# Performance work log

Hardware: AMD Instinct MI355X
Metric: run time of the kernel (lower is better)

The kernel has to match this reference:

```python
import jax, jax.numpy as jnp
import numpy as np

N, L, HH, WW, E, NH = 8, 300, 96, 96, 256, 8


def setup_inputs() -> dict:
    key = jax.random.key(0)
    ks = jax.random.split(key, 9)
    return {
        "query_row": jax.random.normal(ks[0], (N, L, E), dtype=jnp.float32),
        "query_col": jax.random.normal(ks[1], (N, L, E), dtype=jnp.float32),
        "key_row": jax.random.normal(ks[2], (N, HH, WW, E), dtype=jnp.float32),
        "key_col": jax.random.normal(ks[3], (N, HH, WW, E), dtype=jnp.float32),
        "value": jax.random.normal(ks[4], (N, HH, WW, E), dtype=jnp.float32),
        "in_proj_weight": jax.random.normal(ks[5], (5 * E, E), dtype=jnp.float32) * 0.02,
        "in_proj_bias": jax.random.normal(ks[6], (5 * E,), dtype=jnp.float32) * 0.02,
        "out_proj_weight": jax.random.normal(ks[7], (E, E), dtype=jnp.float32) * 0.02,
        "out_proj_bias": jax.random.normal(ks[8], (E,), dtype=jnp.float32) * 0.02,
        "num_heads": NH,
    }


def reference(query_row, query_col, key_row, key_col, value,
              in_proj_weight, in_proj_bias, out_proj_weight, out_proj_bias,
              num_heads):
    bsz, tgt_len, embed_dim = query_row.shape
    head_dim = embed_dim // num_heads
    scaling = float(head_dim) ** -0.5

    def proj(x, i):
        w = in_proj_weight[i * embed_dim:(i + 1) * embed_dim]
        b = in_proj_bias[i * embed_dim:(i + 1) * embed_dim]
        return x @ w.T + b

    q_row = proj(query_row, 0) * scaling          # (N, L, E)
    q_col = proj(query_col, 1) * scaling          # (N, L, E)
    k_row = proj(key_row, 2).mean(axis=1)         # mean over H -> (N, W, E)
    k_col = proj(key_col, 3).mean(axis=2)         # mean over W -> (N, H, E)
    v = proj(value, 4)                            # (N, H, W, E)

    heads = lambda t: t.reshape(*t.shape[:-1], num_heads, head_dim)
    qr, qc, kr, kc = heads(q_row), heads(q_col), heads(k_row), heads(k_col)
    vh = heads(v)                                 # (N, H, W, nh, hd)

    # additive row/col decomposed scores -> independent softmaxes
    w_row = jax.nn.softmax(jnp.einsum('blnd,bwnd->bnlw', qr, kr), axis=-1)  # (N,nh,L,W)
    w_col = jax.nn.softmax(jnp.einsum('blnd,bhnd->bnlh', qc, kc), axis=-1)  # (N,nh,L,H)

    # contract col weights with value over H, then row weights over W
    tmp = jnp.einsum('bnlh,bhwnd->bnlwd', w_col, vh)       # (N,nh,L,W,hd)
    out = jnp.einsum('bnlw,bnlwd->blnd', w_row, tmp)       # (N,L,nh,hd)
    out = out.reshape(bsz, tgt_len, embed_dim).transpose(1, 0, 2)  # (L,N,E)
    return out @ out_proj_weight.T + out_proj_bias
```

## Files before the change

kernel.cpp:

```cpp
#include <hip/hip_runtime.h>
#include <cstdint>


typedef __attribute__((ext_vector_type(8))) short short8v;
typedef __attribute__((ext_vector_type(4))) short short4v;
typedef __attribute__((ext_vector_type(4))) float f32x4;

#define SCALE_Q 0.17677669529663687f

#define GLL16(gp, lp)                                                   \
  __builtin_amdgcn_global_load_lds(                                     \
      (const __attribute__((address_space(1))) void*)(gp),              \
      (__attribute__((address_space(3))) void*)(lp), 16, 0, 0)

__device__ __forceinline__ unsigned short f2bf(float x) {
  unsigned int u = __builtin_bit_cast(unsigned int, x);
  u += 0x7FFFu + ((u >> 16) & 1u);
  return (unsigned short)(u >> 16);
}

__device__ __forceinline__ unsigned int cvtpk(float a, float b) {
  unsigned int r;
  asm("v_cvt_pk_bf16_f32 %0, %1, %2" : "=v"(r) : "v"(a), "v"(b));
  return r;
}

__device__ __forceinline__ short8v pack8cvt(const f32x4& lo, const f32x4& hi) {
  union { short8v s; unsigned int u[4]; } z;
  z.u[0] = cvtpk(lo[0], lo[1]);
  z.u[1] = cvtpk(lo[2], lo[3]);
  z.u[2] = cvtpk(hi[0], hi[1]);
  z.u[3] = cvtpk(hi[2], hi[3]);
  return z.s;
}

__device__ __forceinline__ short4v pack4cvt(float a, float b, float c, float d) {
  union { short4v s; unsigned int u[2]; } z;
  z.u[0] = cvtpk(a, b);
  z.u[1] = cvtpk(c, d);
  return z.s;
}

__device__ __forceinline__ short8v pack8(const float4& fa, const float4& fb) {
  short8v v;
  v[0] = (short)f2bf(fa.x); v[1] = (short)f2bf(fa.y);
  v[2] = (short)f2bf(fa.z); v[3] = (short)f2bf(fa.w);
  v[4] = (short)f2bf(fb.x); v[5] = (short)f2bf(fb.y);
  v[6] = (short)f2bf(fb.z); v[7] = (short)f2bf(fb.w);
  return v;
}

__global__ __launch_bounds__(256) void cvt_w_kernel(const float* __restrict__ w_in,
                                                    const float* __restrict__ w_out,
                                                    short* __restrict__ Wb) {
  int idx = blockIdx.x * 256 + threadIdx.x;
  float v = (idx < 327680) ? w_in[idx] : w_out[idx - 327680];
  Wb[idx] = (short)f2bf(v);
}

__global__ __launch_bounds__(256) void mean_over_h_v3(const float* __restrict__ in,
                                                      float* __restrict__ out) {
  __shared__ float4 part[256];
  int bw = blockIdx.x;
  int b = bw / 96, w = bw - b * 96;
  int t = threadIdx.x, e4 = t & 63, hq = t >> 6;
  const float4* p = (const float4*)(in + ((size_t)b * 9216 + w) * 256) + e4 +
                    (size_t)hq * 24 * 6144;
  float4 s = {0.f, 0.f, 0.f, 0.f};
#pragma unroll
  for (int i = 0; i < 24; ++i) {
    float4 v = p[(size_t)i * 6144];
    s.x += v.x; s.y += v.y; s.z += v.z; s.w += v.w;
  }
  part[t] = s;
  __syncthreads();
  if (t < 64) {
    float4 a = part[t], c = part[t + 64], d = part[t + 128], e = part[t + 192];
    float4 o;
    o.x = (a.x + c.x + d.x + e.x) * (1.f / 96.f);
    o.y = (a.y + c.y + d.y + e.y) * (1.f / 96.f);
    o.z = (a.z + c.z + d.z + e.z) * (1.f / 96.f);
    o.w = (a.w + c.w + d.w + e.w) * (1.f / 96.f);
    ((float4*)out)[(size_t)bw * 64 + t] = o;
  }
}

__global__ __launch_bounds__(256) void mean_over_w_v3(const float* __restrict__ in,
                                                      float* __restrict__ out) {
  __shared__ float4 part[256];
  int bh = blockIdx.x;
  int t = threadIdx.x, e4 = t & 63, wq = t >> 6;
  const float4* p = (const float4*)(in + (size_t)bh * 24576) + e4 + (size_t)wq * 24 * 64;
  float4 s = {0.f, 0.f, 0.f, 0.f};
#pragma unroll
  for (int i = 0; i < 24; ++i) {
    float4 v = p[(size_t)i * 64];
    s.x += v.x; s.y += v.y; s.z += v.z; s.w += v.w;
  }
  part[t] = s;
  __syncthreads();
  if (t < 64) {
    float4 a = part[t], c = part[t + 64], d = part[t + 128], e = part[t + 192];
    float4 o;
    o.x = (a.x + c.x + d.x + e.x) * (1.f / 96.f);
    o.y = (a.y + c.y + d.y + e.y) * (1.f / 96.f);
    o.z = (a.z + c.z + d.z + e.z) * (1.f / 96.f);
    o.w = (a.w + c.w + d.w + e.w) * (1.f / 96.f);
    ((float4*)out)[(size_t)bh * 64 + t] = o;
  }
}

__global__ __launch_bounds__(256) void gemm_proj(
    const float* __restrict__ A0, const float* __restrict__ A1,
    const short* __restrict__ Wb, const float* __restrict__ bias,
    float* __restrict__ Cf, short* __restrict__ Cb0, short* __restrict__ Cb1,
    float scale, int mode) {
  __shared__ short As[32 * 264];
  int y = blockIdx.y;
  const float* A = y ? A1 : A0;
  short* Cb = y ? Cb1 : Cb0;
  const short* Wp = Wb + y * 65536;
  const float* bp = bias + y * 256;
  int t = threadIdx.x;
  int m0 = blockIdx.x * 32;
  int wave = t >> 6, lane = t & 63, r = lane & 15, g = lane >> 4;

  {
    int row = t >> 3, c0 = (t & 7) * 32;
    const float* ap = A + ((size_t)m0 + row) * 256 + c0;
    float4 ld[8];
#pragma unroll
    for (int j = 0; j < 8; ++j) ld[j] = *(const float4*)(ap + j * 4);
    short* dst = &As[row * 264 + c0];
#pragma unroll
    for (int j = 0; j < 4; ++j)
      *(short8v*)(dst + j * 8) = pack8(ld[2 * j], ld[2 * j + 1]);
  }
  __syncthreads();

  f32x4 acc[2][4] = {};
  const short* wbase = Wp + (size_t)(wave * 64 + r) * 256;
#pragma unroll
  for (int ks = 0; ks < 8; ++ks) {
    short8v af0 = *(const short8v*)&As[r * 264 + ks * 32 + g * 8];
    short8v af1 = *(const short8v*)&As[(16 + r) * 264 + ks * 32 + g * 8];
    short8v bf[4];
#pragma unroll
    for (int nf = 0; nf < 4; ++nf)
      bf[nf] = *(const short8v*)(wbase + nf * 16 * 256 + ks * 32 + g * 8);
#pragma unroll
    for (int nf = 0; nf < 4; ++nf) {
      acc[0][nf] = __builtin_amdgcn_mfma_f32_16x16x32_bf16(af0, bf[nf], acc[0][nf], 0, 0, 0);
      acc[1][nf] = __builtin_amdgcn_mfma_f32_16x16x32_bf16(af1, bf[nf], acc[1][nf], 0, 0, 0);
    }
  }

#pragma unroll
  for (int mf = 0; mf < 2; ++mf)
#pragma unroll
    for (int nf = 0; nf < 4; ++nf) {
      int nn = wave * 64 + nf * 16 + r;
      float bval = bp[nn];
#pragma unroll
      for (int i = 0; i < 4; ++i) {
        int m = m0 + mf * 16 + g * 4 + i;
        float val = (acc[mf][nf][i] + bval) * scale;
        if (mode == 1) {
          int bb = m / 300, ll = m - bb * 300;
          Cf[((size_t)ll * 8 + bb) * 256 + nn] = val;
        } else {
          Cb[(size_t)m * 256 + nn] = (short)f2bf(val);
        }
      }
    }
}

__global__ __launch_bounds__(512, 4) void vproj_kernel(
    const float* __restrict__ A, const short* __restrict__ Wb,
    const float* __restrict__ bias, short* __restrict__ vvT) {
  __shared__ float buf[2][16 * 260];
  __shared__ short Ts[8][32 * 36];
  int t = threadIdx.x;
  int wave = t >> 6, lane = t & 63, r = lane & 15, g = lane >> 4;
  int m0g = blockIdx.x * 144;
  int b_ = blockIdx.x >> 6;
  int hw00 = (blockIdx.x & 63) * 144;
  int chbase = wave * 32;

  short8v bf[8][2];
  {
    const short* wbase = Wb + (size_t)(chbase + r) * 256;
#pragma unroll
    for (int ks = 0; ks < 8; ++ks)
#pragma unroll
      for (int nf = 0; nf < 2; ++nf)
        bf[ks][nf] = *(const short8v*)(wbase + nf * 16 * 256 + ks * 32 + g * 8);
  }
#pragma unroll
  for (int ks = 0; ks < 8; ++ks)
#pragma unroll
    for (int nf = 0; nf < 2; ++nf)
      asm volatile("" : "+a"(bf[ks][nf]));
  float bias_v[2];
#pragma unroll
  for (int nf = 0; nf < 2; ++nf) bias_v[nf] = bias[chbase + nf * 16 + r];

#pragma unroll
  for (int q = 0; q < 2; ++q) {
#pragma unroll
    for (int i = 0; i < 2; ++i) {
      int row = wave * 2 + i;
      const float* gp = A + ((size_t)m0g + q * 16 + row) * 256 + lane * 4;
      GLL16(gp, &buf[q][row * 260]);
    }
  }

  int chg = chbase + (lane & 31);
  int half = lane >> 5;
  short* vbase = vvT + (size_t)(b_ * 8 + (chg >> 5)) * 294912 +
                 (size_t)(chg & 31) * 9216 + hw00;
  const short* tsr = &Ts[wave][(lane & 31) * 36];

#pragma unroll
  for (int tt = 0; tt < 9; ++tt) {
    if (tt == 0 || (tt & 1) || tt == 8)
      asm volatile("s_waitcnt vmcnt(2)" ::: "memory");
    else
      asm volatile("s_waitcnt vmcnt(4)" ::: "memory");
    __builtin_amdgcn_s_barrier();

    f32x4 acc[2] = {};
    const float* bp_ = &buf[tt & 1][0];
#pragma unroll
    for (int ks = 0; ks < 8; ++ks) {
      const float* p = bp_ + r * 260 + ks * 32 + g * 8;
      f32x4 lo = *(const f32x4*)p;
      f32x4 hi = *(const f32x4*)(p + 4);
      short8v af = pack8cvt(lo, hi);
      acc[0] = __builtin_amdgcn_mfma_f32_16x16x32_bf16(af, bf[ks][0], acc[0], 0, 0, 0);
      acc[1] = __builtin_amdgcn_mfma_f32_16x16x32_bf16(af, bf[ks][1], acc[1], 0, 0, 0);
    }

#pragma unroll
    for (int nf = 0; nf < 2; ++nf) {
      float bv = bias_v[nf];
      *(short4v*)&Ts[wave][(nf * 16 + r) * 36 + (tt & 1) * 16 + g * 4] =
          pack4cvt(acc[nf][0] + bv, acc[nf][1] + bv, acc[nf][2] + bv, acc[nf][3] + bv);
    }
    asm volatile("" ::: "memory");

    if (tt & 1) {
      short* gdst = vbase + (tt - 1) * 16 + half * 16;
      const short* src = tsr + half * 16;
      *(short8v*)gdst = *(const short8v*)src;
      *(short8v*)(gdst + 8) = *(const short8v*)(src + 8);
      asm volatile("" ::: "memory");
    }

    __builtin_amdgcn_s_barrier();
    if (tt + 2 < 9) {
#pragma unroll
      for (int i = 0; i < 2; ++i) {
        int row = wave * 2 + i;
        const float* gp = A + ((size_t)m0g + (tt + 2) * 16 + row) * 256 + lane * 4;
        GLL16(gp, &buf[tt & 1][row * 260]);
      }
    }
  }
  {
    short* gdst = vbase + 128 + half * 8;
    *(short8v*)gdst = *(const short8v*)(tsr + half * 8);
  }
}

__global__ __launch_bounds__(64) void scores_softmax_v2(
    const short* __restrict__ qrb, const short* __restrict__ qcb,
    const short* __restrict__ krb, const short* __restrict__ kcb,
    short* __restrict__ wrowB, float* __restrict__ wcolT) {
  int lchunk = blockIdx.x, bn = blockIdx.y, kind = blockIdx.z;
  int b = bn >> 3, n = bn & 7;
  int lane = threadIdx.x;
  int r = lane & 15, g = lane >> 4;
  const short* qb = kind ? qcb : qrb;
  const short* kb = kind ? kcb : krb;
  int l0 = lchunk * 80;

  short8v a[5], bfr[6];
#pragma unroll
  for (int lf = 0; lf < 5; ++lf) {
    int l = l0 + lf * 16 + r;
    if (l > 299) l = 299;
    a[lf] = *(const short8v*)(qb + ((size_t)b * 300 + l) * 256 + n * 32 + g * 8);
  }
#pragma unroll
  for (int f = 0; f < 6; ++f)
    bfr[f] = *(const short8v*)(kb + ((size_t)b * 96 + f * 16 + r) * 256 + n * 32 + g * 8);

  f32x4 c[5][6];
#pragma unroll
  for (int lf = 0; lf < 5; ++lf)
#pragma unroll
    for (int f = 0; f < 6; ++f) {
      f32x4 z = {};
      c[lf][f] = __builtin_amdgcn_mfma_f32_16x16x32_bf16(a[lf], bfr[f], z, 0, 0, 0);
    }

#pragma unroll
  for (int lf = 0; lf < 5; ++lf)
#pragma unroll
    for (int i = 0; i < 4; ++i) {
      float m = c[lf][0][i];
#pragma unroll
      for (int f = 1; f < 6; ++f) m = fmaxf(m, c[lf][f][i]);
#pragma unroll
      for (int mask = 1; mask <= 8; mask <<= 1) m = fmaxf(m, __shfl_xor(m, mask, 64));
      float e[6], s = 0.f;
#pragma unroll
      for (int f = 0; f < 6; ++f) { e[f] = __expf(c[lf][f][i] - m); s += e[f]; }
#pragma unroll
      for (int mask = 1; mask <= 8; mask <<= 1) s += __shfl_xor(s, mask, 64);
      float inv = 1.f / s;
#pragma unroll
      for (int f = 0; f < 6; ++f) c[lf][f][i] = e[f] * inv;
    }

  if (kind == 0) {
#pragma unroll
    for (int lf = 0; lf < 5; ++lf)
#pragma unroll
      for (int i = 0; i < 4; ++i) {
        int l = l0 + lf * 16 + g * 4 + i;
        bool ok = (l < 300);
#pragma unroll
        for (int f = 0; f < 6; ++f) {
          float wv = ok ? c[lf][f][i] : 0.f;
          wrowB[((size_t)bn * 320 + l) * 96 + f * 16 + r] = (short)f2bf(wv);
        }
      }
  } else {
#pragma unroll
    for (int lf = 0; lf < 5; ++lf)
#pragma unroll
      for (int f = 0; f < 6; ++f) {
        int l = l0 + lf * 16 + g * 4;
        f32x4 wv = c[lf][f];
#pragma unroll
        for (int i = 0; i < 4; ++i) if (l + i >= 300) wv[i] = 0.f;
        *(f32x4*)(wcolT + ((size_t)bn * 96 + f * 16 + r) * 320 + l) = wv;
      }
  }
}

__global__ __launch_bounds__(512, 2) void attn_kernel(
    const short* __restrict__ wrowB, const float* __restrict__ wcolT,
    const short* __restrict__ vvT, float* __restrict__ ao) {
  __shared__ f32x4 cmb[3][2][4][64];
  int i = blockIdx.x;
  int xcd = i & 7, j = i >> 3;
  int bn = (j / 5) * 8 + xcd;
  int lh = j - (j / 5) * 5;
  int b = bn >> 3, n = bn & 7;
  int t = threadIdx.x, wave = t >> 6, lane = t & 63;
  int df = wave & 1, hh = wave >> 1;
  int lbase = lh * 64;
  int r = lane & 15, g = lane >> 4;

  short8v a[4][3];
  const short* wr = wrowB + (size_t)bn * 320 * 96;
#pragma unroll
  for (int lf = 0; lf < 4; ++lf)
#pragma unroll
    for (int ks = 0; ks < 3; ++ks)
      a[lf][ks] = *(const short8v*)(wr + (lbase + lf * 16 + r) * 96 + ks * 32 + g * 8);

  const short* vb = vvT + (size_t)bn * 294912 + (size_t)(df * 16 + r) * 9216 + hh * 24 * 96;
  const float* wcb = wcolT + ((size_t)bn * 96 + hh * 24) * 320 + lbase + g * 4;

  f32x4 acc[4] = {};
  short8v bR[4][3];
  f32x4 wR[4][4];
#pragma unroll
  for (int q = 0; q < 4; ++q) {
#pragma unroll
    for (int ks = 0; ks < 3; ++ks)
      bR[q][ks] = *(const short8v*)(vb + q * 96 + ks * 32 + g * 8);
#pragma unroll
    for (int lf = 0; lf < 4; ++lf)
      wR[q][lf] = *(const f32x4*)(wcb + q * 320 + lf * 16);
  }
  asm volatile("" ::: "memory");

#pragma unroll
  for (int hs = 0; hs < 24; ++hs) {
    int cur = hs & 3;
    f32x4 R[4] = {};
#pragma unroll
    for (int ks = 0; ks < 3; ++ks)
#pragma unroll
      for (int lf = 0; lf < 4; ++lf)
        R[lf] = __builtin_amdgcn_mfma_f32_16x16x32_bf16(a[lf][ks], bR[cur][ks], R[lf], 0, 0, 0);
#pragma unroll
    for (int lf = 0; lf < 4; ++lf) acc[lf] += wR[cur][lf] * R[lf];
    if (hs + 4 < 24) {
#pragma unroll
      for (int ks = 0; ks < 3; ++ks)
        bR[cur][ks] = *(const short8v*)(vb + (hs + 4) * 96 + ks * 32 + g * 8);
#pragma unroll
      for (int lf = 0; lf < 4; ++lf)
        wR[cur][lf] = *(const f32x4*)(wcb + (hs + 4) * 320 + lf * 16);
    }
    asm volatile("" ::: "memory");
  }

  if (hh > 0) {
#pragma unroll
    for (int lf = 0; lf < 4; ++lf) cmb[hh - 1][df][lf][lane] = acc[lf];
  }
  __syncthreads();
  if (hh == 0) {
#pragma unroll
    for (int lf = 0; lf < 4; ++lf) {
      f32x4 o = acc[lf];
#pragma unroll
      for (int q = 0; q < 3; ++q) o += cmb[q][df][lf][lane];
#pragma unroll
      for (int i2 = 0; i2 < 4; ++i2) {
        int l = lbase + lf * 16 + g * 4 + i2;
        if (l < 300)
          ao[((size_t)b * 300 + l) * 256 + n * 32 + df * 16 + r] = o[i2];
      }
    }
  }
}

extern "C" void kernel_launch(void* const* d_in, const int* in_sizes, int n_in,
                              void* d_out, int out_size, void* d_ws, size_t ws_size,
                              hipStream_t stream) {
  const float* query_row = (const float*)d_in[0];
  const float* query_col = (const float*)d_in[1];
  const float* key_row   = (const float*)d_in[2];
  const float* key_col   = (const float*)d_in[3];
  const float* value     = (const float*)d_in[4];
  const float* W         = (const float*)d_in[5];
  const float* Bv        = (const float*)d_in[6];
  const float* Wout      = (const float*)d_in[7];
  const float* Bout      = (const float*)d_in[8];

  float* ws = (float*)d_ws;
  float* krm   = ws;
  float* kcm   = krm + 196608;
  float* ao    = kcm + 196608;
  float* wcolT = ao + 614400;
  short* qrb   = (short*)(wcolT + 1966080);
  short* qcb   = qrb + 614400;
  short* krb   = qcb + 614400;
  short* kcb   = krb + 196608;
  short* wrowB = kcb + 196608;
  short* vvT   = wrowB + 1966080;
  short* Wb    = vvT + 18874368;

  cvt_w_kernel<<<1536, 256, 0, stream>>>(W, Wout, Wb);
  mean_over_h_v3<<<768, 256, 0, stream>>>(key_row, krm);
  mean_over_w_v3<<<768, 256, 0, stream>>>(key_col, kcm);
  gemm_proj<<<dim3(75, 2), 256, 0, stream>>>(query_row, query_col, Wb, Bv,
                                             nullptr, qrb, qcb, SCALE_Q, 3);
  gemm_proj<<<dim3(24, 2), 256, 0, stream>>>(krm, kcm, Wb + 131072, Bv + 512,
                                             nullptr, krb, kcb, 1.f, 3);
  vproj_kernel<<<512, 512, 0, stream>>>(value, Wb + 262144, Bv + 1024, vvT);
  scores_softmax_v2<<<dim3(4, 64, 2), 64, 0, stream>>>(qrb, qcb, krb, kcb, wrowB, wcolT);
  attn_kernel<<<320, 512, 0, stream>>>(wrowB, wcolT, vvT, ao);
  gemm_proj<<<dim3(75, 1), 256, 0, stream>>>(ao, nullptr, Wb + 327680, Bout,
                                             (float*)d_out, nullptr, nullptr, 1.f, 1);
}
```

Measured before the change: 155.9 us.

## Split attention over H across blocks with partial buffers and separate reduce kernel

The attention kernel is repartitioned so that each block handles one (batch, head) pair and one eighth of H (12 rows), with its 8 waves covering all 320 L rows. This replaces the old split, where each block covered 64 L rows across all of H and waves reduced partials in shared memory. Per-block partial sums go to a global partial buffer and a new reduce kernel adds the 8 H-slices into the attention output. The aim is to raise the block count from 320 to 512 for better CU occupancy and to shorten the prefetch pipeline to double buffering. The cost is about 20 MB of extra global writes and reads plus one more kernel launch.

Measured after the change: 198.1 us. +27.0%, slower.

```diff
diff --git a/kernel.cpp b/kernel.cpp
--- a/kernel.cpp
+++ b/kernel.cpp
@@ -351,86 +351,86 @@
   }
 }
 
-__global__ __launch_bounds__(512, 2) void attn_kernel(
+__global__ __launch_bounds__(512, 2) void attn_v3(
     const short* __restrict__ wrowB, const float* __restrict__ wcolT,
-    const short* __restrict__ vvT, float* __restrict__ ao) {
-  __shared__ f32x4 cmb[3][2][4][64];
+    const short* __restrict__ vvT, float* __restrict__ part) {
   int i = blockIdx.x;
   int xcd = i & 7, j = i >> 3;
-  int bn = (j / 5) * 8 + xcd;
-  int lh = j - (j / 5) * 5;
+  int bn = ((j & 7) << 3) + xcd;
+  int hq = j >> 3;
+  int t = threadIdx.x, wave = t >> 6, lane = t & 63;
+  int df = wave & 1, lq = wave >> 1;
+  int l0 = lq * 80;
+  int r = lane & 15, g = lane >> 4;
+
+  short8v a[5][3];
+  const short* wr = wrowB + (size_t)bn * 320 * 96;
+#pragma unroll
+  for (int lf = 0; lf < 5; ++lf)
+#pragma unroll
+    for (int ks = 0; ks < 3; ++ks)
+      a[lf][ks] = *(const short8v*)(wr + (l0 + lf * 16 + r) * 96 + ks * 32 + g * 8);
+
+  const short* vb = vvT + (size_t)bn * 294912 + (size_t)(df * 16 + r) * 9216 +
+                    hq * 12 * 96;
+  const float* wcb = wcolT + ((size_t)bn * 96 + hq * 12) * 320 + l0 + g * 4;
+
+  f32x4 acc[5] = {};
+  short8v bR[2][3];
+  f32x4 wR[2][5];
+#pragma unroll
+  for (int ks = 0; ks < 3; ++ks) bR[0][ks] = *(const short8v*)(vb + ks * 32 + g * 8);
+#pragma unroll
+  for (int lf = 0; lf < 5; ++lf) wR[0][lf] = *(const f32x4*)(wcb + lf * 16);
+  asm volatile("" ::: "memory");
+
+#pragma unroll
+  for (int hs = 0; hs < 12; ++hs) {
+    int cur = hs & 1, nxt = cur ^ 1;
+    if (hs < 11) {
+#pragma unroll
+      for (int ks = 0; ks < 3; ++ks)
+        bR[nxt][ks] = *(const short8v*)(vb + (hs + 1) * 96 + ks * 32 + g * 8);
+#pragma unroll
+      for (int lf = 0; lf < 5; ++lf)
+        wR[nxt][lf] = *(const f32x4*)(wcb + (hs + 1) * 320 + lf * 16);
+    }
+    f32x4 R[5] = {};
+#pragma unroll
+    for (int ks = 0; ks < 3; ++ks)
+#pragma unroll
+      for (int lf = 0; lf < 5; ++lf)
+        R[lf] = __builtin_amdgcn_mfma_f32_16x16x32_bf16(a[lf][ks], bR[cur][ks], R[lf], 0, 0, 0);
+#pragma unroll
+    for (int lf = 0; lf < 5; ++lf) acc[lf] += wR[cur][lf] * R[lf];
+    asm volatile("" ::: "memory");
+  }
+
+  float* pb = part + ((size_t)(hq * 64 + bn) * 320) * 32 + df * 16 + r;
+#pragma unroll
+  for (int lf = 0; lf < 5; ++lf)
+#pragma unroll
+    for (int i2 = 0; i2 < 4; ++i2) {
+      int l = l0 + lf * 16 + g * 4 + i2;
+      pb[(size_t)l * 32] = acc[lf][i2];
+      pb += 0;
+    }
+}
+
+
+__global__ __launch_bounds__(256) void reduce_kernel(const float* __restrict__ part,
+                                                     float* __restrict__ ao) {
+  int idx = blockIdx.x * 256 + threadIdx.x;
+  int d = idx & 31;
+  int rest = idx >> 5;
+  int l = rest % 300;
+  int bn = rest / 300;
+  float s = 0.f;
+#pragma unroll
+  for (int hq = 0; hq < 8; ++hq)
+    s += part[((size_t)(hq * 64 + bn) * 320 + l) * 32 + d];
   int b = bn >> 3, n = bn & 7;
-  int t = threadIdx.x, wave = t >> 6, lane = t & 63;
-  int df = wave & 1, hh = wave >> 1;
-  int lbase = lh * 64;
-  int r = lane & 15, g = lane >> 4;
-
-  short8v a[4][3];
-  const short* wr = wrowB + (size_t)bn * 320 * 96;
-#pragma unroll
-  for (int lf = 0; lf < 4; ++lf)
-#pragma unroll
-    for (int ks = 0; ks < 3; ++ks)
-      a[lf][ks] = *(const short8v*)(wr + (lbase + lf * 16 + r) * 96 + ks * 32 + g * 8);
-
-  const short* vb = vvT + (size_t)bn * 294912 + (size_t)(df * 16 + r) * 9216 + hh * 24 * 96;
-  const float* wcb = wcolT + ((size_t)bn * 96 + hh * 24) * 320 + lbase + g * 4;
-
-  f32x4 acc[4] = {};
-  short8v bR[4][3];
-  f32x4 wR[4][4];
-#pragma unroll
-  for (int q = 0; q < 4; ++q) {
-#pragma unroll
-    for (int ks = 0; ks < 3; ++ks)
-      bR[q][ks] = *(const short8v*)(vb + q * 96 + ks * 32 + g * 8);
-#pragma unroll
-    for (int lf = 0; lf < 4; ++lf)
-      wR[q][lf] = *(const f32x4*)(wcb + q * 320 + lf * 16);
-  }
-  asm volatile("" ::: "memory");
-
-#pragma unroll
-  for (int hs = 0; hs < 24; ++hs) {
-    int cur = hs & 3;
-    f32x4 R[4] = {};
-#pragma unroll
-    for (int ks = 0; ks < 3; ++ks)
-#pragma unroll
-      for (int lf = 0; lf < 4; ++lf)
-        R[lf] = __builtin_amdgcn_mfma_f32_16x16x32_bf16(a[lf][ks], bR[cur][ks], R[lf], 0, 0, 0);
-#pragma unroll
-    for (int lf = 0; lf < 4; ++lf) acc[lf] += wR[cur][lf] * R[lf];
-    if (hs + 4 < 24) {
-#pragma unroll
-      for (int ks = 0; ks < 3; ++ks)
-        bR[cur][ks] = *(const short8v*)(vb + (hs + 4) * 96 + ks * 32 + g * 8);
-#pragma unroll
-      for (int lf = 0; lf < 4; ++lf)
-        wR[cur][lf] = *(const f32x4*)(wcb + (hs + 4) * 320 + lf * 16);
-    }
-    asm volatile("" ::: "memory");
-  }
-
-  if (hh > 0) {
-#pragma unroll
-    for (int lf = 0; lf < 4; ++lf) cmb[hh - 1][df][lf][lane] = acc[lf];
-  }
-  __syncthreads();
-  if (hh == 0) {
-#pragma unroll
-    for (int lf = 0; lf < 4; ++lf) {
-      f32x4 o = acc[lf];
-#pragma unroll
-      for (int q = 0; q < 3; ++q) o += cmb[q][df][lf][lane];
-#pragma unroll
-      for (int i2 = 0; i2 < 4; ++i2) {
-        int l = lbase + lf * 16 + g * 4 + i2;
-        if (l < 300)
-          ao[((size_t)b * 300 + l) * 256 + n * 32 + df * 16 + r] = o[i2];
-      }
-    }
-  }
+  ao[((size_t)b * 300 + l) * 256 + n * 32 + d] = s;
 }
 
 extern "C" void kernel_launch(void* const* d_in, const int* in_sizes, int n_in,
@@ -451,7 +451,8 @@
   float* kcm   = krm + 196608;
   float* ao    = kcm + 196608;
   float* wcolT = ao + 614400;
-  short* qrb   = (short*)(wcolT + 1966080);
+  float* part  = wcolT + 1966080;
+  short* qrb   = (short*)(part + 5242880);
   short* qcb   = qrb + 614400;
   short* krb   = qcb + 614400;
   short* kcb   = krb + 196608;
@@ -468,7 +469,8 @@
                                              nullptr, krb, kcb, 1.f, 3);
   vproj_kernel<<<512, 512, 0, stream>>>(value, Wb + 262144, Bv + 1024, vvT);
   scores_softmax_v2<<<dim3(4, 64, 2), 64, 0, stream>>>(qrb, qcb, krb, kcb, wrowB, wcolT);
-  attn_kernel<<<320, 512, 0, stream>>>(wrowB, wcolT, vvT, ao);
+  attn_v3<<<512, 512, 0, stream>>>(wrowB, wcolT, vvT, part);
+  reduce_kernel<<<2400, 256, 0, stream>>>(part, ao);
   gemm_proj<<<dim3(75, 1), 256, 0, stream>>>(ao, nullptr, Wb + 327680, Bout,
                                              (float*)d_out, nullptr, nullptr, 1.f, 1);
 }
```
